# Kernel tuning notes

Measured on AMD Instinct MI355X. Metric: run time of the kernel, lower is better.

## Reference

```python
import jax, jax.numpy as jnp
import numpy as np

EPS = 1e-6  # F.pairwise_distance default eps, added to the difference


def setup_inputs() -> dict:
    key = jax.random.key(0)
    k1, k2 = jax.random.split(key)
    N, NS, NQ, D = 2048, 5, 8, 256
    x = jax.random.normal(k1, (N, NS + NQ, D), dtype=jnp.float32)
    label = jax.random.randint(k2, (N,), 0, N, dtype=jnp.int64)
    return {"x": x, "label": label, "n_s": NS, "n_q": NQ}


def reference(x, label, n_s, n_q):
    # x: [N, n_s+n_q, D]
    anchors = jnp.mean(x[:, :n_s, :], axis=1)               # [N, D] prototypes
    N, D = anchors.shape
    queries = x[:, n_s:n_s + n_q, :].reshape(N * n_q, D)     # [N*n_q, D]

    # Exact ||q - a + eps||^2 via GEMM expansion (matches F.pairwise_distance(.,.)**2):
    # ||q-a||^2 + 2*eps*sum(q-a) + D*eps^2
    q_sq = jnp.sum(queries * queries, axis=-1)               # [N*n_q]
    a_sq = jnp.sum(anchors * anchors, axis=-1)               # [N]
    cross = queries @ anchors.T                              # [N*n_q, N]
    q_sum = jnp.sum(queries, axis=-1)                        # [N*n_q]
    a_sum = jnp.sum(anchors, axis=-1)                        # [N]
    dist_sq = (q_sq[:, None] + a_sq[None, :] - 2.0 * cross
               + 2.0 * EPS * (q_sum[:, None] - a_sum[None, :])
               + D * EPS * EPS)
    logits = -dist_sq                                        # [N*n_q, N]

    lab = jnp.repeat(label, n_q)                             # [N*n_q]
    logp = jax.nn.log_softmax(logits, axis=-1)
    nloss = -jnp.mean(jnp.take_along_axis(logp, lab[:, None], axis=1))
    prec1 = jnp.mean((jnp.argmax(logits, axis=-1) == lab).astype(jnp.float32)) * 100.0
    return nloss, prec1
```

## Files before the change

### kernel.cpp

```cpp
#include <hip/hip_runtime.h>
#include <math.h>

#define EPS  1e-6f
#define DD   256
#define NSUP 5
#define NQ   8
#define SEQ  13
#define L2E  1.44269504088896f
#define LN2  0.693147180559945f
#define NEP  2048
#define NROW 16384
#define NCOL 2048

typedef short bf16x8 __attribute__((ext_vector_type(8)));
typedef unsigned short u16x4 __attribute__((ext_vector_type(4)));
typedef float f32x4  __attribute__((ext_vector_type(4)));

__device__ __forceinline__ ushort f2bf(float f) {
  union { float f; unsigned u; } v; v.f = f;
  unsigned r = v.u + 0x7FFFu + ((v.u >> 16) & 1u);
  return (ushort)(r >> 16);
}
__device__ __forceinline__ float bf2f(short u) {
  union { unsigned u; float f; } v; v.u = ((unsigned)(unsigned short)u) << 16;
  return v.f;
}

__global__ __launch_bounds__(256) void proto_prep(
    const float* __restrict__ x, float* __restrict__ cb,
    ushort* __restrict__ Asw, ushort* __restrict__ Qsw,
    float* __restrict__ accum, int* __restrict__ fincount) {
  const int tid = threadIdx.x, g = tid >> 6, l = tid & 63;
  const int n = blockIdx.x * 4 + g;
  if (blockIdx.x == 0 && tid == 0) { accum[0] = 0.f; accum[1] = 0.f; fincount[0] = 0; }

  const float4* xr4 = (const float4*)(x + (size_t)n * SEQ * DD);

  const int d0   = l * 4;
  const int kk   = d0 >> 5, quad = (d0 >> 3) & 3, j = d0 & 7;
  const size_t chunk_d = (size_t)kk * 64 + (size_t)quad * 16;

  float4 a = {0.f, 0.f, 0.f, 0.f};
  #pragma unroll
  for (int s = 0; s < NSUP; ++s) {
    float4 v = xr4[s * 64 + l];
    a.x += v.x; a.y += v.y; a.z += v.z; a.w += v.w;
  }
  a.x *= 0.2f; a.y *= 0.2f; a.z *= 0.2f; a.w *= 0.2f;
  {
    const size_t idx = (((size_t)(n >> 4) * 8) * 64 + chunk_d + (n & 15)) * 8 + j;
    u16x4 o = {f2bf(a.x), f2bf(a.y), f2bf(a.z), f2bf(a.w)};
    *(u16x4*)(Asw + idx) = o;
  }
  float s1 = a.x + a.y + a.z + a.w;
  float s2 = a.x * a.x + a.y * a.y + a.z * a.z + a.w * a.w;
  #pragma unroll
  for (int off = 32; off; off >>= 1) {
    s1 += __shfl_xor(s1, off);
    s2 += __shfl_xor(s2, off);
  }
  if (l == 0) cb[n] = -L2E * (s2 - 2.f * EPS * s1);

  #pragma unroll
  for (int s = 0; s < NQ; ++s) {
    float4 q = xr4[(NSUP + s) * 64 + l];
    const int row = n * NQ + s;
    const size_t idx = (((size_t)(row >> 4) * 8) * 64 + chunk_d + (row & 15)) * 8 + j;
    u16x4 o = {f2bf(q.x), f2bf(q.y), f2bf(q.z), f2bf(q.w)};
    *(u16x4*)(Qsw + idx) = o;
  }
}

__global__ __launch_bounds__(512, 1) void proto_main(
    const ushort* __restrict__ Qsw, const ushort* __restrict__ Asw,
    const float* __restrict__ cb, const int* __restrict__ label,
    float* __restrict__ partm, float* __restrict__ parts,
    int* __restrict__ partbi, float* __restrict__ slabws) {
  const int tid  = threadIdx.x;
  const int wid  = tid >> 6, lane = tid & 63;
  const int quad = lane >> 4, lcol = lane & 15;
  const int rowg = wid & 3, colg = wid >> 2;
  const int rb   = blockIdx.x & 63;
  const int colc = blockIdx.x >> 6;
  const int r0   = rb * 256;

  const bf16x8* qb = (const bf16x8*)Qsw;
  const bf16x8* bb = (const bf16x8*)Asw;

  __shared__ bf16x8 Bl[2][2][8][64];
  __shared__ float  sCb[512];

  sCb[tid] = cb[colc * 512 + tid];

  bf16x8 af[4][8];
  #pragma unroll
  for (int set = 0; set < 4; ++set) {
    const size_t base = ((size_t)(rb * 16 + rowg * 4 + set) * 8) * 64 + lane;
    #pragma unroll
    for (int kk = 0; kk < 8; ++kk) af[set][kk] = qb[base + (size_t)kk * 64];
  }

  float m[4][4], s[4][4];
  int   bi[4][4];
  #pragma unroll
  for (int set = 0; set < 4; ++set)
    #pragma unroll
    for (int i = 0; i < 4; ++i) {
      m[set][i] = -1e30f; s[set][i] = 0.f; bi[set][i] = 0x7fffffff;
    }

  const int kk0 = rowg * 2;
  auto stage = [&](int tl, int b) {
    const int T = colc * 32 + colg * 16 + tl;
    #pragma unroll
    for (int k2 = 0; k2 < 2; ++k2) {
      const int kk = kk0 + k2;
      const ushort* src = Asw + (((size_t)T * 8 + kk) * 64 + lane) * 8;
      __builtin_amdgcn_global_load_lds(
          (const __attribute__((address_space(1))) void*)src,
          (__attribute__((address_space(3))) void*)&Bl[colg][b][kk][0],
          16, 0, 0);
    }
  };

  auto compute = [&](int tl, int b) {
    f32x4 c0 = {0.f, 0.f, 0.f, 0.f}, c1 = {0.f, 0.f, 0.f, 0.f};
    f32x4 c2 = {0.f, 0.f, 0.f, 0.f}, c3 = {0.f, 0.f, 0.f, 0.f};
    #pragma unroll
    for (int kk = 0; kk < 8; ++kk) {
      bf16x8 bf = Bl[colg][b][kk][lane];
      c0 = __builtin_amdgcn_mfma_f32_16x16x32_bf16(af[0][kk], bf, c0, 0, 0, 0);
      c1 = __builtin_amdgcn_mfma_f32_16x16x32_bf16(af[1][kk], bf, c1, 0, 0, 0);
      c2 = __builtin_amdgcn_mfma_f32_16x16x32_bf16(af[2][kk], bf, c2, 0, 0, 0);
      c3 = __builtin_amdgcn_mfma_f32_16x16x32_bf16(af[3][kk], bf, c3, 0, 0, 0);
    }
    const int   lcIdx  = (colg * 16 + tl) * 16 + lcol;
    const int   colIdx = colc * 512 + lcIdx;
    const float cbv    = sCb[lcIdx];
    #pragma unroll
    for (int set = 0; set < 4; ++set) {
      #pragma unroll
      for (int i = 0; i < 4; ++i) {
        float cv = (set == 0) ? c0[i] : (set == 1) ? c1[i]
                 : (set == 2) ? c2[i] : c3[i];
        float v2 = fmaf(cv, 2.f * L2E, cbv);
        float dv = v2 - m[set][i];
        bool  gt = dv > 0.f;
        float e  = exp2f(-fabsf(dv));
        s[set][i]  = fmaf(s[set][i], gt ? e : 1.f, gt ? 1.f : e);
        m[set][i]  = fmaxf(m[set][i], v2);
        bi[set][i] = gt ? colIdx : bi[set][i];
      }
    }
  };

  stage(0, 0);
  __syncthreads();

  #pragma unroll 1
  for (int t = 0; t < 16; t += 2) {
    stage(t + 1, 1);
    compute(t, 0);
    __syncthreads();
    if (t + 2 < 16) stage(t + 2, 0);
    compute(t + 1, 1);
    __syncthreads();
  }

  #pragma unroll
  for (int mask = 1; mask < 16; mask <<= 1) {
    #pragma unroll
    for (int set = 0; set < 4; ++set)
      #pragma unroll
      for (int i = 0; i < 4; ++i) {
        float om = __shfl_xor(m[set][i], mask);
        float os = __shfl_xor(s[set][i], mask);
        int   oi = __shfl_xor(bi[set][i], mask);
        float nm = fmaxf(m[set][i], om);
        s[set][i] = s[set][i] * exp2f(m[set][i] - nm) + os * exp2f(om - nm);
        bool better = (om > m[set][i]) || (om == m[set][i] && oi < bi[set][i]);
        bi[set][i] = better ? oi : bi[set][i];
        m[set][i]  = nm;
      }
  }

  __shared__ float sm[2][256], ssh[2][256];
  __shared__ int   sbi[2][256];
  if (lcol == 0) {
    #pragma unroll
    for (int set = 0; set < 4; ++set)
      #pragma unroll
      for (int i = 0; i < 4; ++i) {
        int rl = rowg * 64 + set * 16 + quad * 4 + i;
        sm[colg][rl] = m[set][i]; ssh[colg][rl] = s[set][i]; sbi[colg][rl] = bi[set][i];
      }
  }
  __syncthreads();

  if (tid < 256) {
    float mm = sm[0][tid], sv = ssh[0][tid];
    int   b  = sbi[0][tid];
    {
      float om = sm[1][tid], os = ssh[1][tid];
      int   oi = sbi[1][tid];
      float nm = fmaxf(mm, om);
      sv = sv * exp2f(mm - nm) + os * exp2f(om - nm);
      bool better = (om > mm) || (om == mm && oi < b);
      b = better ? oi : b;
      mm = nm;
    }
    const int row = r0 + tid;
    partm [colc * NROW + row] = mm;
    parts [colc * NROW + row] = sv;
    partbi[colc * NROW + row] = b;
  }

  if (colc == 0) {
    const int rl = tid >> 1, l = tid & 1;
    const int row = r0 + rl;
    const int lab = label[row >> 3];
    float dot = 0.f;
    #pragma unroll
    for (int c = 0; c < 4; ++c) {
      const int kk = l * 4 + c;
      const size_t qc = ((size_t)(row >> 4) * 8 + kk) * 64 + (row & 15);
      const size_t ac = ((size_t)(lab >> 4) * 8 + kk) * 64 + (lab & 15);
      #pragma unroll
      for (int qd = 0; qd < 4; ++qd) {
        bf16x8 qv = qb[qc + qd * 16];
        bf16x8 av = bb[ac + qd * 16];
        #pragma unroll
        for (int j = 0; j < 8; ++j) dot = fmaf(bf2f(qv[j]), bf2f(av[j]), dot);
      }
    }
    dot += __shfl_xor(dot, 1);
    if (l == 0) slabws[row] = fmaf(dot, 2.f * L2E, cb[lab]);
  }
}

__global__ __launch_bounds__(256) void proto_merge(
    const float* __restrict__ partm, const float* __restrict__ parts,
    const int* __restrict__ partbi, const float* __restrict__ slabws,
    const int* __restrict__ label,
    float* __restrict__ accum, int* __restrict__ fincount,
    float* __restrict__ out) {
  const int tid = threadIdx.x, row = blockIdx.x * 256 + tid;
  const int wid = tid >> 6;

  float mm = partm[row], sv = parts[row];
  int   b  = partbi[row];
  #pragma unroll
  for (int c = 1; c < 4; ++c) {
    float om = partm[c * NROW + row], os = parts[c * NROW + row];
    int   oi = partbi[c * NROW + row];
    float nm = fmaxf(mm, om);
    sv = sv * exp2f(mm - nm) + os * exp2f(om - nm);
    bool better = (om > mm) || (om == mm && oi < b);
    b = better ? oi : b;
    mm = nm;
  }

  const int lb = label[row >> 3];
  float loss = LN2 * (mm + log2f(sv) - slabws[row]);
  float corr = (b == lb) ? 1.f : 0.f;

  #pragma unroll
  for (int mask = 32; mask; mask >>= 1) {
    loss += __shfl_xor(loss, mask);
    corr += __shfl_xor(corr, mask);
  }
  __shared__ float red[2][4];
  if ((tid & 63) == 0) { red[0][wid] = loss; red[1][wid] = corr; }
  __syncthreads();
  if (tid == 0) {
    float L = red[0][0] + red[0][1] + red[0][2] + red[0][3];
    float C = red[1][0] + red[1][1] + red[1][2] + red[1][3];
    atomicAdd(&accum[0], L);
    atomicAdd(&accum[1], C);
    __threadfence();
    if (atomicAdd(fincount, 1) == (int)gridDim.x - 1) {
      out[0] = atomicAdd(&accum[0], 0.f) / (float)NROW;
      out[1] = atomicAdd(&accum[1], 0.f) * 100.f / (float)NROW;
    }
  }
}

extern "C" void kernel_launch(void* const* d_in, const int* in_sizes, int n_in,
                              void* d_out, int out_size, void* d_ws, size_t ws_size,
                              hipStream_t stream) {
  const float* x     = (const float*)d_in[0];
  const int*   label = (const int*)d_in[1];
  float* out = (float*)d_out;

  float*  W        = (float*)d_ws;
  float*  accum    = W;
  int*    fincount = (int*)(W + 2);
  float*  cb       = W + 16;
  ushort* Asw      = (ushort*)(cb + NCOL);
  ushort* Qsw      = Asw + (size_t)NCOL * DD;
  float*  partm    = (float*)(Qsw + (size_t)NROW * DD);
  float*  parts    = partm + 4 * NROW;
  int*    partbi   = (int*)(parts + 4 * NROW);
  float*  slabws   = (float*)(partbi + 4 * NROW);

  hipLaunchKernelGGL(proto_prep, dim3(NEP / 4), dim3(256), 0, stream,
                     x, cb, Asw, Qsw, accum, fincount);
  hipLaunchKernelGGL(proto_main, dim3(256), dim3(512), 0, stream,
                     Qsw, Asw, cb, label, partm, parts, partbi, slabws);
  hipLaunchKernelGGL(proto_merge, dim3(NROW / 256), dim3(256), 0, stream,
                     partm, parts, partbi, slabws, label, accum, fincount, out);
}
```

Before: 121.2 us.

## Split main GEMM-softmax kernel into 512 smaller blocks with 8 column chunks

Restructures proto_main from 256 blocks of 512 threads (two column groups merged in shared memory) into 512 blocks of 256 threads, each covering 256 columns. The in-block cross-group merge and its barrier are removed, and partials are written straight to global memory, with the merge kernel now combining 8 partials per row instead of 4. This is meant to fill more CUs on the MI355X and allow two blocks per CU, at the cost of twice as much partial-result traffic and each block reloading its full Q tile into registers.

```diff
diff --git a/kernel.cpp b/kernel.cpp
--- a/kernel.cpp
+++ b/kernel.cpp
@@ -71,15 +71,14 @@
   }
 }
 
-__global__ __launch_bounds__(512, 1) void proto_main(
+__global__ __launch_bounds__(256, 2) void proto_main(
     const ushort* __restrict__ Qsw, const ushort* __restrict__ Asw,
     const float* __restrict__ cb, const int* __restrict__ label,
     float* __restrict__ partm, float* __restrict__ parts,
     int* __restrict__ partbi, float* __restrict__ slabws) {
   const int tid  = threadIdx.x;
-  const int wid  = tid >> 6, lane = tid & 63;
+  const int rowg = tid >> 6, lane = tid & 63;
   const int quad = lane >> 4, lcol = lane & 15;
-  const int rowg = wid & 3, colg = wid >> 2;
   const int rb   = blockIdx.x & 63;
   const int colc = blockIdx.x >> 6;
   const int r0   = rb * 256;
@@ -87,10 +86,10 @@
   const bf16x8* qb = (const bf16x8*)Qsw;
   const bf16x8* bb = (const bf16x8*)Asw;
 
-  __shared__ bf16x8 Bl[2][2][8][64];
-  __shared__ float  sCb[512];
-
-  sCb[tid] = cb[colc * 512 + tid];
+  __shared__ bf16x8 Bl[2][8][64];
+  __shared__ float  sCb[256];
+
+  sCb[tid] = cb[colc * 256 + tid];
 
   bf16x8 af[4][8];
   #pragma unroll
@@ -111,14 +110,14 @@
 
   const int kk0 = rowg * 2;
   auto stage = [&](int tl, int b) {
-    const int T = colc * 32 + colg * 16 + tl;
+    const int T = colc * 16 + tl;
     #pragma unroll
     for (int k2 = 0; k2 < 2; ++k2) {
       const int kk = kk0 + k2;
       const ushort* src = Asw + (((size_t)T * 8 + kk) * 64 + lane) * 8;
       __builtin_amdgcn_global_load_lds(
           (const __attribute__((address_space(1))) void*)src,
-          (__attribute__((address_space(3))) void*)&Bl[colg][b][kk][0],
+          (__attribute__((address_space(3))) void*)&Bl[b][kk][0],
           16, 0, 0);
     }
   };
@@ -128,14 +127,14 @@
     f32x4 c2 = {0.f, 0.f, 0.f, 0.f}, c3 = {0.f, 0.f, 0.f, 0.f};
     #pragma unroll
     for (int kk = 0; kk < 8; ++kk) {
-      bf16x8 bf = Bl[colg][b][kk][lane];
+      bf16x8 bf = Bl[b][kk][lane];
       c0 = __builtin_amdgcn_mfma_f32_16x16x32_bf16(af[0][kk], bf, c0, 0, 0, 0);
       c1 = __builtin_amdgcn_mfma_f32_16x16x32_bf16(af[1][kk], bf, c1, 0, 0, 0);
       c2 = __builtin_amdgcn_mfma_f32_16x16x32_bf16(af[2][kk], bf, c2, 0, 0, 0);
       c3 = __builtin_amdgcn_mfma_f32_16x16x32_bf16(af[3][kk], bf, c3, 0, 0, 0);
     }
-    const int   lcIdx  = (colg * 16 + tl) * 16 + lcol;
-    const int   colIdx = colc * 512 + lcIdx;
+    const int   lcIdx  = tl * 16 + lcol;
+    const int   colIdx = colc * 256 + lcIdx;
     const float cbv    = sCb[lcIdx];
     #pragma unroll
     for (int set = 0; set < 4; ++set) {
@@ -184,45 +183,24 @@
       }
   }
 
-  __shared__ float sm[2][256], ssh[2][256];
-  __shared__ int   sbi[2][256];
   if (lcol == 0) {
     #pragma unroll
     for (int set = 0; set < 4; ++set)
       #pragma unroll
       for (int i = 0; i < 4; ++i) {
-        int rl = rowg * 64 + set * 16 + quad * 4 + i;
-        sm[colg][rl] = m[set][i]; ssh[colg][rl] = s[set][i]; sbi[colg][rl] = bi[set][i];
-      }
-  }
-  __syncthreads();
-
-  if (tid < 256) {
-    float mm = sm[0][tid], sv = ssh[0][tid];
-    int   b  = sbi[0][tid];
-    {
-      float om = sm[1][tid], os = ssh[1][tid];
-      int   oi = sbi[1][tid];
-      float nm = fmaxf(mm, om);
-      sv = sv * exp2f(mm - nm) + os * exp2f(om - nm);
-      bool better = (om > mm) || (om == mm && oi < b);
-      b = better ? oi : b;
-      mm = nm;
-    }
+        const int row = r0 + rowg * 64 + set * 16 + quad * 4 + i;
+        partm [colc * NROW + row] = m[set][i];
+        parts [colc * NROW + row] = s[set][i];
+        partbi[colc * NROW + row] = bi[set][i];
+      }
+  }
+
+  if (colc == 0) {
     const int row = r0 + tid;
-    partm [colc * NROW + row] = mm;
-    parts [colc * NROW + row] = sv;
-    partbi[colc * NROW + row] = b;
-  }
-
-  if (colc == 0) {
-    const int rl = tid >> 1, l = tid & 1;
-    const int row = r0 + rl;
     const int lab = label[row >> 3];
     float dot = 0.f;
     #pragma unroll
-    for (int c = 0; c < 4; ++c) {
-      const int kk = l * 4 + c;
+    for (int kk = 0; kk < 8; ++kk) {
       const size_t qc = ((size_t)(row >> 4) * 8 + kk) * 64 + (row & 15);
       const size_t ac = ((size_t)(lab >> 4) * 8 + kk) * 64 + (lab & 15);
       #pragma unroll
@@ -233,8 +211,7 @@
         for (int j = 0; j < 8; ++j) dot = fmaf(bf2f(qv[j]), bf2f(av[j]), dot);
       }
     }
-    dot += __shfl_xor(dot, 1);
-    if (l == 0) slabws[row] = fmaf(dot, 2.f * L2E, cb[lab]);
+    slabws[row] = fmaf(dot, 2.f * L2E, cb[lab]);
   }
 }
 
@@ -250,7 +227,7 @@
   float mm = partm[row], sv = parts[row];
   int   b  = partbi[row];
   #pragma unroll
-  for (int c = 1; c < 4; ++c) {
+  for (int c = 1; c < 8; ++c) {
     float om = partm[c * NROW + row], os = parts[c * NROW + row];
     int   oi = partbi[c * NROW + row];
     float nm = fmaxf(mm, om);
@@ -299,13 +276,13 @@
   ushort* Asw      = (ushort*)(cb + NCOL);
   ushort* Qsw      = Asw + (size_t)NCOL * DD;
   float*  partm    = (float*)(Qsw + (size_t)NROW * DD);
-  float*  parts    = partm + 4 * NROW;
-  int*    partbi   = (int*)(parts + 4 * NROW);
-  float*  slabws   = (float*)(partbi + 4 * NROW);
+  float*  parts    = partm + 8 * NROW;
+  int*    partbi   = (int*)(parts + 8 * NROW);
+  float*  slabws   = (float*)(partbi + 8 * NROW);
 
   hipLaunchKernelGGL(proto_prep, dim3(NEP / 4), dim3(256), 0, stream,
                      x, cb, Asw, Qsw, accum, fincount);
-  hipLaunchKernelGGL(proto_main, dim3(256), dim3(512), 0, stream,
+  hipLaunchKernelGGL(proto_main, dim3(512), dim3(256), 0, stream,
                      Qsw, Asw, cb, label, partm, parts, partbi, slabws);
   hipLaunchKernelGGL(proto_merge, dim3(NROW / 256), dim3(256), 0, stream,
                      partm, parts, partbi, slabws, label, accum, fincount, out);
```

Measured after the change: 120.8 us. No clear change (-0.3%).
